# Kernel optimization log

Measured on AMD Instinct MI355X. Metric: run time of the kernel, lower is better.

Reference implementation:

```python
import jax, jax.numpy as jnp
import numpy as np

B, L, D = 16, 2048, 128
GROUP = 16
NG = L // GROUP  # number of groups per batch
ALPHA = 0.5


def setup_inputs() -> dict:
    key = jax.random.key(0)
    k0, k1, k2 = jax.random.split(key, 3)
    x = jax.random.normal(k0, (B, L, D), dtype=jnp.float32)
    # per-batch permutation = gather indices (each position used exactly once)
    group_tensor = jax.vmap(lambda k: jax.random.permutation(k, L))(
        jax.random.split(k1, B)).astype(jnp.int32)
    ctxlens = jnp.full((B,), L, dtype=jnp.int32)
    W = jax.random.normal(k2, (2 * D,), dtype=jnp.float32) * (1.0 / np.sqrt(D))
    norm_alpha = jnp.ones((2,), dtype=jnp.float32)
    norm_gamma = jnp.ones((2 * D,), dtype=jnp.float32)
    norm_beta = jnp.zeros((2 * D,), dtype=jnp.float32)
    return {"x": x, "group_tensor": group_tensor, "ctxlens": ctxlens, "W": W,
            "norm_alpha": norm_alpha, "norm_gamma": norm_gamma, "norm_beta": norm_beta}


def _leaky_relu(v):
    return jnp.where(v >= 0, v, 0.01 * v)


def _ncn_forward(x, group_tensor, ctxlens, W, norm_alpha, norm_gamma, norm_beta):
    Bd, Ld, Dd = x.shape
    ng = Ld // GROUP
    Wi, Wj = W[:Dd], W[Dd:]
    a1, a2 = norm_alpha[0], norm_alpha[1]
    g1, g2 = norm_gamma[:Dd], norm_gamma[Dd:]
    b1, b2 = norm_beta[:Dd], norm_beta[Dd:]

    # gather x by group indices -> [B, NG, GROUP, D]
    xg = jnp.take_along_axis(x, group_tensor[:, :, None].astype(jnp.int32), axis=1)
    xg = xg.reshape(Bd, ng, GROUP, Dd)

    def step(carry, j):
        xi, xa = carry  # each [B, NG, GROUP, D]
        xj = jax.lax.dynamic_slice_in_dim(xi, j, 1, axis=2)  # [B, NG, 1, D]
        sim = jnp.einsum('bgnd,d->bgn', xi, Wi) \
            + jnp.einsum('bgd,d->bg', xj[:, :, 0, :], Wj)[:, :, None]  # [B,NG,GROUP]
        T = ALPHA * xi + (1.0 - ALPHA) * sim[..., None] * xj
        T_norm = g1 * jnp.tanh(a1 * T) + b1
        Fv = _leaky_relu(T_norm)
        xa = xa + Fv                               # ya = xa + F
        xi = xi + g2 * jnp.tanh(a2 * xa) + b2      # yi = xi + norm2(ya)
        return (xi, xa), None

    (yi, ya), _ = jax.lax.scan(step, (xg, jnp.zeros_like(xg)), jnp.arange(GROUP))

    # kernel only processes/stores a group if its start offset < ctxlen
    valid = (jnp.arange(ng, dtype=jnp.int32) * GROUP)[None, :] < ctxlens[:, None]
    yi = jnp.where(valid[:, :, None, None], yi, 0.0).reshape(Bd, Ld, Dd)
    ya = jnp.where(valid[:, :, None, None], ya, 0.0).reshape(Bd, Ld, Dd)

    # scatter back to original positions
    bidx = jnp.arange(Bd)[:, None]
    yi_out = jnp.zeros_like(x).at[bidx, group_tensor].set(yi)
    ya_out = jnp.zeros_like(x).at[bidx, group_tensor].set(ya)
    return yi_out, ya_out


def reference(x, group_tensor, ctxlens, W, norm_alpha, norm_gamma, norm_beta):
    return _ncn_forward(x, group_tensor, ctxlens, W, norm_alpha, norm_gamma, norm_beta)
```

## Files before the change

### kernel.cpp

```cpp
#include <hip/hip_runtime.h>

#define B_ 16
#define L_ 2048
#define D_ 128
#define GROUP_ 16
#define NG_ (L_ / GROUP_)
#define LOG2E_ 1.44269504088896340736f

typedef float v2 __attribute__((ext_vector_type(2)));

template<int CTRL>
__device__ __forceinline__ float dpp_add(float v) {
    int x = __builtin_amdgcn_update_dpp(0, __float_as_int(v), CTRL, 0xF, 0xF, false);
    return v + __int_as_float(x);
}
__device__ __forceinline__ float row16_sum(float v) {
    v = dpp_add<0xB1>(v);
    v = dpp_add<0x4E>(v);
    v = dpp_add<0x141>(v);
    v = dpp_add<0x140>(v);
    return v;
}

#define STEP_LOOP(SELFN)                                                      \
    for (int j = 0; j < GROUP_; ++j) {                                        \
        const int p = j & 1;                                                  \
        v2 xjv[4];                                                            \
        {                                                                     \
            float4 tA = *(const float4*)&s_xj[p][d0];                         \
            float4 tB = *(const float4*)&s_xj[p][d0 + 4];                     \
            xjv[0] = (v2){tA.x, tA.y}; xjv[1] = (v2){tA.z, tA.w};             \
            xjv[2] = (v2){tB.x, tB.y}; xjv[3] = (v2){tB.z, tB.w};             \
        }                                                                     \
        v2 sv = (v2){0.0f, 0.0f};                                             \
        _Pragma("unroll")                                                     \
        for (int k = 0; k < 4; ++k) sv = __builtin_elementwise_fma(cxi[k], Wi[k], sv); \
        _Pragma("unroll")                                                     \
        for (int k = 0; k < 4; ++k) sv = __builtin_elementwise_fma(xjv[k], Wj[k], sv); \
        const float sim = row16_sum(sv.x + sv.y);                             \
        const v2 simv = (v2){sim, sim};                                       \
        _Pragma("unroll")                                                     \
        for (int k = 0; k < 4; ++k) {                                         \
            v2 u  = __builtin_elementwise_fma(simv, xjv[k], cxi[k]);          \
            v2 r1 = (v2){__builtin_amdgcn_rcpf(__builtin_amdgcn_exp2f(u.x) + 1.0f),   \
                         __builtin_amdgcn_rcpf(__builtin_amdgcn_exp2f(u.y) + 1.0f)};  \
            v2 tnS = __builtin_elementwise_fma(G1S[k], r1, B1S[k]);           \
            v2 FvS = SELFN(tnS, tnS * leak);                                  \
            za[k] += FvS;                                                     \
            v2 r2 = (v2){__builtin_amdgcn_rcpf(__builtin_amdgcn_exp2f(za[k].x) + 1.0f), \
                         __builtin_amdgcn_rcpf(__builtin_amdgcn_exp2f(za[k].y) + 1.0f)}; \
            cxi[k] = __builtin_elementwise_fma(G2c[k], r2, cxi[k] + B2c[k]);  \
        }                                                                     \
        if (j + 1 < GROUP_ && row == j + 1) {                                 \
            *(v2*)&s_xj[p ^ 1][d0]     = cxi[0];                              \
            *(v2*)&s_xj[p ^ 1][d0 + 2] = cxi[1];                              \
            *(v2*)&s_xj[p ^ 1][d0 + 4] = cxi[2];                              \
            *(v2*)&s_xj[p ^ 1][d0 + 6] = cxi[3];                              \
        }                                                                     \
        __syncthreads();                                                      \
    }

__global__ __launch_bounds__(256, 4) void ncn_kernel(
    const float* __restrict__ x,
    const int*   __restrict__ gt,
    const int*   __restrict__ ctxlens,
    const float* __restrict__ W,
    const float* __restrict__ nalpha,
    const float* __restrict__ ngamma,
    const float* __restrict__ nbeta,
    float* __restrict__ out)
{
    const int blk = blockIdx.x;
    const int b   = blk >> 7;
    const int g   = blk & (NG_ - 1);
    const int tid = threadIdx.x;
    const int row = tid >> 4;
    const int rl  = tid & 15;
    const int d0  = rl << 3;

    __shared__ float s_xj[2][D_];

    const float a1 = nalpha[0];
    const float a2 = nalpha[1];
    const float ca = -a1 * LOG2E_;
    const float S  = -2.0f * a2 * LOG2E_;
    const float inv_ca = 1.0f / ca;
    const bool  selMin = (S < 0.0f);

    v2 Wi[4], Wj[4], G1S[4], B1S[4], G2c[4], B2c[4];
    {
        float4 wA = *(const float4*)(W + d0);
        float4 wB = *(const float4*)(W + d0 + 4);
        float4 vA = *(const float4*)(W + D_ + d0);
        float4 vB = *(const float4*)(W + D_ + d0 + 4);
        Wi[0] = inv_ca * (v2){wA.x, wA.y}; Wi[1] = inv_ca * (v2){wA.z, wA.w};
        Wi[2] = inv_ca * (v2){wB.x, wB.y}; Wi[3] = inv_ca * (v2){wB.z, wB.w};
        Wj[0] = inv_ca * (v2){vA.x, vA.y}; Wj[1] = inv_ca * (v2){vA.z, vA.w};
        Wj[2] = inv_ca * (v2){vB.x, vB.y}; Wj[3] = inv_ca * (v2){vB.z, vB.w};

        float4 g1A = *(const float4*)(ngamma + d0);
        float4 g1B = *(const float4*)(ngamma + d0 + 4);
        float4 g2A = *(const float4*)(ngamma + D_ + d0);
        float4 g2B = *(const float4*)(ngamma + D_ + d0 + 4);
        float4 b1A = *(const float4*)(nbeta + d0);
        float4 b1B = *(const float4*)(nbeta + d0 + 4);
        float4 b2A = *(const float4*)(nbeta + D_ + d0);
        float4 b2B = *(const float4*)(nbeta + D_ + d0 + 4);

        v2 g1v[4] = {(v2){g1A.x,g1A.y},(v2){g1A.z,g1A.w},(v2){g1B.x,g1B.y},(v2){g1B.z,g1B.w}};
        v2 b1v[4] = {(v2){b1A.x,b1A.y},(v2){b1A.z,b1A.w},(v2){b1B.x,b1B.y},(v2){b1B.z,b1B.w}};
        v2 g2v[4] = {(v2){g2A.x,g2A.y},(v2){g2A.z,g2A.w},(v2){g2B.x,g2B.y},(v2){g2B.z,g2B.w}};
        v2 b2v[4] = {(v2){b2A.x,b2A.y},(v2){b2A.z,b2A.w},(v2){b2B.x,b2B.y},(v2){b2B.z,b2B.w}};
#pragma unroll
        for (int k = 0; k < 4; ++k) {
            G1S[k] = (S * 2.0f) * g1v[k];
            B1S[k] = S * (b1v[k] - g1v[k]);
            G2c[k] = (ca * 2.0f) * g2v[k];
            B2c[k] = ca * (b2v[k] - g2v[k]);
        }
    }

    const int l   = g * GROUP_ + row;
    const int tok = gt[b * L_ + l];
    const float* xp = x + ((size_t)(b * L_ + tok)) * D_ + d0;

    v2 cxi[4], za[4];
    {
        float4 xA = *(const float4*)xp;
        float4 xB = *(const float4*)(xp + 4);
        const v2 cav = (v2){ca, ca};
        cxi[0] = cav * (v2){xA.x, xA.y}; cxi[1] = cav * (v2){xA.z, xA.w};
        cxi[2] = cav * (v2){xB.x, xB.y}; cxi[3] = cav * (v2){xB.z, xB.w};
    }
#pragma unroll
    for (int k = 0; k < 4; ++k) za[k] = (v2){0.0f, 0.0f};

    if (row == 0) {
        *(v2*)&s_xj[0][d0]     = cxi[0];
        *(v2*)&s_xj[0][d0 + 2] = cxi[1];
        *(v2*)&s_xj[0][d0 + 4] = cxi[2];
        *(v2*)&s_xj[0][d0 + 6] = cxi[3];
    }
    __syncthreads();

    const v2 leak = (v2){0.01f, 0.01f};

    if (selMin) {
        STEP_LOOP(__builtin_elementwise_min)
    } else {
        STEP_LOOP(__builtin_elementwise_max)
    }

    const float invS = 1.0f / S;
    const v2 invSv  = (v2){invS, invS};
    const v2 invCav = (v2){inv_ca, inv_ca};
    v2 xi[4], xa[4];
#pragma unroll
    for (int k = 0; k < 4; ++k) {
        xi[k] = cxi[k] * invCav;
        xa[k] = za[k] * invSv;
    }

    const bool valid = (g * GROUP_) < ctxlens[b];
    if (!valid) {
#pragma unroll
        for (int k = 0; k < 4; ++k) { xi[k] = (v2){0,0}; xa[k] = (v2){0,0}; }
    }

    float* o1 = out + ((size_t)(b * L_ + tok)) * D_ + d0;
    float* o2 = o1 + (size_t)B_ * L_ * D_;
    float4 s1A = {xi[0].x, xi[0].y, xi[1].x, xi[1].y};
    float4 s1B = {xi[2].x, xi[2].y, xi[3].x, xi[3].y};
    float4 s2A = {xa[0].x, xa[0].y, xa[1].x, xa[1].y};
    float4 s2B = {xa[2].x, xa[2].y, xa[3].x, xa[3].y};
    *(float4*)o1       = s1A;
    *(float4*)(o1 + 4) = s1B;
    *(float4*)o2       = s2A;
    *(float4*)(o2 + 4) = s2B;
}

extern "C" void kernel_launch(void* const* d_in, const int* in_sizes, int n_in,
                              void* d_out, int out_size, void* d_ws, size_t ws_size,
                              hipStream_t stream) {
    const float* x  = (const float*)d_in[0];
    const int*   gt = (const int*)d_in[1];
    const int*   cl = (const int*)d_in[2];
    const float* W  = (const float*)d_in[3];
    const float* na = (const float*)d_in[4];
    const float* ng = (const float*)d_in[5];
    const float* nb = (const float*)d_in[6];
    float* out = (float*)d_out;

    ncn_kernel<<<B_ * NG_, 256, 0, stream>>>(x, gt, cl, W, na, ng, nb, out);
}
```

Baseline: 111.9 us.

## Move per-channel constants to LDS and raise occupancy target

Measured after the change: 135.9 us. 1.21x slower.

```diff
diff --git a/kernel.cpp b/kernel.cpp
--- a/kernel.cpp
+++ b/kernel.cpp
@@ -22,15 +22,25 @@
     return v;
 }
 
+#define LGKM_BARRIER() asm volatile("s_waitcnt lgkmcnt(0)\n\ts_barrier" ::: "memory")
+
 #define STEP_LOOP(SELFN)                                                      \
     for (int j = 0; j < GROUP_; ++j) {                                        \
         const int p = j & 1;                                                  \
-        v2 xjv[4];                                                            \
+        v2 xjv[4], Wi[4], Wj[4];                                              \
         {                                                                     \
             float4 tA = *(const float4*)&s_xj[p][d0];                         \
             float4 tB = *(const float4*)&s_xj[p][d0 + 4];                     \
             xjv[0] = (v2){tA.x, tA.y}; xjv[1] = (v2){tA.z, tA.w};             \
             xjv[2] = (v2){tB.x, tB.y}; xjv[3] = (v2){tB.z, tB.w};             \
+            float4 wA = *(const float4*)(cbase + 0 * D_ + d0);                \
+            float4 wB = *(const float4*)(cbase + 0 * D_ + d0 + 4);            \
+            float4 vA = *(const float4*)(cbase + 1 * D_ + d0);                \
+            float4 vB = *(const float4*)(cbase + 1 * D_ + d0 + 4);            \
+            Wi[0] = (v2){wA.x, wA.y}; Wi[1] = (v2){wA.z, wA.w};               \
+            Wi[2] = (v2){wB.x, wB.y}; Wi[3] = (v2){wB.z, wB.w};               \
+            Wj[0] = (v2){vA.x, vA.y}; Wj[1] = (v2){vA.z, vA.w};               \
+            Wj[2] = (v2){vB.x, vB.y}; Wj[3] = (v2){vB.z, vB.w};               \
         }                                                                     \
         v2 sv = (v2){0.0f, 0.0f};                                             \
         _Pragma("unroll")                                                     \
@@ -39,28 +49,49 @@
         for (int k = 0; k < 4; ++k) sv = __builtin_elementwise_fma(xjv[k], Wj[k], sv); \
         const float sim = row16_sum(sv.x + sv.y);                             \
         const v2 simv = (v2){sim, sim};                                       \
+        v2 G1S[4], B1S[4], G2c[4], B2c[4];                                    \
+        {                                                                     \
+            float4 aA = *(const float4*)(cbase + 2 * D_ + d0);                \
+            float4 aB = *(const float4*)(cbase + 2 * D_ + d0 + 4);            \
+            float4 bA = *(const float4*)(cbase + 3 * D_ + d0);                \
+            float4 bB = *(const float4*)(cbase + 3 * D_ + d0 + 4);            \
+            float4 cA = *(const float4*)(cbase + 4 * D_ + d0);                \
+            float4 cB = *(const float4*)(cbase + 4 * D_ + d0 + 4);            \
+            float4 dA = *(const float4*)(cbase + 5 * D_ + d0);                \
+            float4 dB = *(const float4*)(cbase + 5 * D_ + d0 + 4);            \
+            G1S[0] = (v2){aA.x, aA.y}; G1S[1] = (v2){aA.z, aA.w};             \
+            G1S[2] = (v2){aB.x, aB.y}; G1S[3] = (v2){aB.z, aB.w};             \
+            B1S[0] = (v2){bA.x, bA.y}; B1S[1] = (v2){bA.z, bA.w};             \
+            B1S[2] = (v2){bB.x, bB.y}; B1S[3] = (v2){bB.z, bB.w};             \
+            G2c[0] = (v2){cA.x, cA.y}; G2c[1] = (v2){cA.z, cA.w};             \
+            G2c[2] = (v2){cB.x, cB.y}; G2c[3] = (v2){cB.z, cB.w};             \
+            B2c[0] = (v2){dA.x, dA.y}; B2c[1] = (v2){dA.z, dA.w};             \
+            B2c[2] = (v2){dB.x, dB.y}; B2c[3] = (v2){dB.z, dB.w};             \
+        }                                                                     \
         _Pragma("unroll")                                                     \
         for (int k = 0; k < 4; ++k) {                                         \
             v2 u  = __builtin_elementwise_fma(simv, xjv[k], cxi[k]);          \
-            v2 r1 = (v2){__builtin_amdgcn_rcpf(__builtin_amdgcn_exp2f(u.x) + 1.0f),   \
-                         __builtin_amdgcn_rcpf(__builtin_amdgcn_exp2f(u.y) + 1.0f)};  \
+            v2 e1 = (v2){__builtin_amdgcn_exp2f(u.x), __builtin_amdgcn_exp2f(u.y)}; \
+            v2 d1 = e1 + onev;                                                \
+            v2 r1 = (v2){__builtin_amdgcn_rcpf(d1.x), __builtin_amdgcn_rcpf(d1.y)}; \
             v2 tnS = __builtin_elementwise_fma(G1S[k], r1, B1S[k]);           \
             v2 FvS = SELFN(tnS, tnS * leak);                                  \
             za[k] += FvS;                                                     \
-            v2 r2 = (v2){__builtin_amdgcn_rcpf(__builtin_amdgcn_exp2f(za[k].x) + 1.0f), \
-                         __builtin_amdgcn_rcpf(__builtin_amdgcn_exp2f(za[k].y) + 1.0f)}; \
+            v2 e2 = (v2){__builtin_amdgcn_exp2f(za[k].x), __builtin_amdgcn_exp2f(za[k].y)}; \
+            v2 d2 = e2 + onev;                                                \
+            v2 r2 = (v2){__builtin_amdgcn_rcpf(d2.x), __builtin_amdgcn_rcpf(d2.y)}; \
             cxi[k] = __builtin_elementwise_fma(G2c[k], r2, cxi[k] + B2c[k]);  \
         }                                                                     \
         if (j + 1 < GROUP_ && row == j + 1) {                                 \
-            *(v2*)&s_xj[p ^ 1][d0]     = cxi[0];                              \
-            *(v2*)&s_xj[p ^ 1][d0 + 2] = cxi[1];                              \
-            *(v2*)&s_xj[p ^ 1][d0 + 4] = cxi[2];                              \
-            *(v2*)&s_xj[p ^ 1][d0 + 6] = cxi[3];                              \
-        }                                                                     \
-        __syncthreads();                                                      \
-    }
-
-__global__ __launch_bounds__(256, 4) void ncn_kernel(
+            float4 oA = {cxi[0].x, cxi[0].y, cxi[1].x, cxi[1].y};             \
+            float4 oB = {cxi[2].x, cxi[2].y, cxi[3].x, cxi[3].y};             \
+            *(float4*)&s_xj[p ^ 1][d0]     = oA;                              \
+            *(float4*)&s_xj[p ^ 1][d0 + 4] = oB;                              \
+        }                                                                     \
+        LGKM_BARRIER();                                                       \
+    }
+
+__global__ __launch_bounds__(256, 6) void ncn_kernel(
     const float* __restrict__ x,
     const int*   __restrict__ gt,
     const int*   __restrict__ ctxlens,
@@ -79,6 +110,7 @@
     const int d0  = rl << 3;
 
     __shared__ float s_xj[2][D_];
+    __shared__ float s_c[6][D_];
 
     const float a1 = nalpha[0];
     const float a2 = nalpha[1];
@@ -87,37 +119,17 @@
     const float inv_ca = 1.0f / ca;
     const bool  selMin = (S < 0.0f);
 
-    v2 Wi[4], Wj[4], G1S[4], B1S[4], G2c[4], B2c[4];
-    {
-        float4 wA = *(const float4*)(W + d0);
-        float4 wB = *(const float4*)(W + d0 + 4);
-        float4 vA = *(const float4*)(W + D_ + d0);
-        float4 vB = *(const float4*)(W + D_ + d0 + 4);
-        Wi[0] = inv_ca * (v2){wA.x, wA.y}; Wi[1] = inv_ca * (v2){wA.z, wA.w};
-        Wi[2] = inv_ca * (v2){wB.x, wB.y}; Wi[3] = inv_ca * (v2){wB.z, wB.w};
-        Wj[0] = inv_ca * (v2){vA.x, vA.y}; Wj[1] = inv_ca * (v2){vA.z, vA.w};
-        Wj[2] = inv_ca * (v2){vB.x, vB.y}; Wj[3] = inv_ca * (v2){vB.z, vB.w};
-
-        float4 g1A = *(const float4*)(ngamma + d0);
-        float4 g1B = *(const float4*)(ngamma + d0 + 4);
-        float4 g2A = *(const float4*)(ngamma + D_ + d0);
-        float4 g2B = *(const float4*)(ngamma + D_ + d0 + 4);
-        float4 b1A = *(const float4*)(nbeta + d0);
-        float4 b1B = *(const float4*)(nbeta + d0 + 4);
-        float4 b2A = *(const float4*)(nbeta + D_ + d0);
-        float4 b2B = *(const float4*)(nbeta + D_ + d0 + 4);
-
-        v2 g1v[4] = {(v2){g1A.x,g1A.y},(v2){g1A.z,g1A.w},(v2){g1B.x,g1B.y},(v2){g1B.z,g1B.w}};
-        v2 b1v[4] = {(v2){b1A.x,b1A.y},(v2){b1A.z,b1A.w},(v2){b1B.x,b1B.y},(v2){b1B.z,b1B.w}};
-        v2 g2v[4] = {(v2){g2A.x,g2A.y},(v2){g2A.z,g2A.w},(v2){g2B.x,g2B.y},(v2){g2B.z,g2B.w}};
-        v2 b2v[4] = {(v2){b2A.x,b2A.y},(v2){b2A.z,b2A.w},(v2){b2B.x,b2B.y},(v2){b2B.z,b2B.w}};
-#pragma unroll
-        for (int k = 0; k < 4; ++k) {
-            G1S[k] = (S * 2.0f) * g1v[k];
-            B1S[k] = S * (b1v[k] - g1v[k]);
-            G2c[k] = (ca * 2.0f) * g2v[k];
-            B2c[k] = ca * (b2v[k] - g2v[k]);
-        }
+    if (tid < D_) {
+        const int d = tid;
+        float w  = W[d],          wj = W[D_ + d];
+        float g1 = ngamma[d],     g2 = ngamma[D_ + d];
+        float b1 = nbeta[d],      b2 = nbeta[D_ + d];
+        s_c[0][d] = w  * inv_ca;
+        s_c[1][d] = wj * inv_ca;
+        s_c[2][d] = (S * 2.0f) * g1;
+        s_c[3][d] = S * (b1 - g1);
+        s_c[4][d] = (ca * 2.0f) * g2;
+        s_c[5][d] = ca * (b2 - g2);
     }
 
     const int l   = g * GROUP_ + row;
@@ -136,13 +148,17 @@
     for (int k = 0; k < 4; ++k) za[k] = (v2){0.0f, 0.0f};
 
     if (row == 0) {
-        *(v2*)&s_xj[0][d0]     = cxi[0];
-        *(v2*)&s_xj[0][d0 + 2] = cxi[1];
-        *(v2*)&s_xj[0][d0 + 4] = cxi[2];
-        *(v2*)&s_xj[0][d0 + 6] = cxi[3];
+        float4 oA = {cxi[0].x, cxi[0].y, cxi[1].x, cxi[1].y};
+        float4 oB = {cxi[2].x, cxi[2].y, cxi[3].x, cxi[3].y};
+        *(float4*)&s_xj[0][d0]     = oA;
+        *(float4*)&s_xj[0][d0 + 4] = oB;
     }
     __syncthreads();
 
+    const float* cbase = &s_c[0][0];
+    asm volatile("" : "+v"(cbase));
+
+    const v2 onev = (v2){1.0f, 1.0f};
     const v2 leak = (v2){0.01f, 0.01f};
 
     if (selMin) {
```
